# Kernel optimization log

Hardware: AMD Instinct MI355X
Metric: run time of the kernel (lower is better)

The kernel has to match this reference:

```python
import jax, jax.numpy as jnp
import numpy as np
from jax import lax


def setup_inputs() -> dict:
    key = jax.random.key(0)
    kx, kw = jax.random.split(key)
    x = jax.random.normal(kx, (8, 32, 16, 160, 160), dtype=jnp.float32)
    # xavier-normal-ish init (scale irrelevant to correctness testing)
    weights = jax.random.normal(kw, (32, 32, 1, 3, 3), dtype=jnp.float32) * 0.1
    return {"x": x, "weights": weights}


def reference(x, weights):
    # per-(out_ch, in_ch) scale: mean |w| over kernel dims (2,3,4), detached
    scale = lax.stop_gradient(jnp.mean(jnp.abs(weights), axis=(2, 3, 4), keepdims=True))
    binary_no_grad = scale * jnp.sign(weights)          # {+-scale}
    clipped = jnp.clip(weights, -1.0, 1.0)
    # straight-through estimator: value = binary_no_grad, grad flows via clipped
    binary_weights = lax.stop_gradient(binary_no_grad - clipped) + clipped
    out = lax.conv_general_dilated(
        x, binary_weights,
        window_strides=(1, 1, 1),
        padding=((0, 0), (1, 1), (1, 1)),
        rhs_dilation=(1, 1, 1),
        dimension_numbers=("NCDHW", "OIDHW", "NCDHW"),
        feature_group_count=1,
    )
    return out
```

## Files before the change

kernel.cpp:

```cpp
#include <hip/hip_runtime.h>
#include <stdint.h>


typedef _Float16 half8  __attribute__((ext_vector_type(8)));
typedef float    floatx4 __attribute__((ext_vector_type(4)));

#define DHW 409600
#define HW  25600
#define RING_SLOT_B 10240
#define RING_B      40960
#define LDS_TOTAL   61440

__device__ __forceinline__ int w1s(int w1) { return w1 ^ ((w1 >> 2) & 1); }
__device__ __forceinline__ int f2v(int w1) { return ((w1 >> 1) ^ (w1 >> 3)) & 3; }

typedef const __attribute__((address_space(1))) uint32_t* gas1;
typedef __attribute__((address_space(3))) uint32_t* las3;
__device__ __forceinline__ void gld16(const void* g, void* l) {
    __builtin_amdgcn_global_load_lds((gas1)g, (las3)l, 16, 0, 0);
}
#define VMCNT(N) do { asm volatile("s_waitcnt vmcnt(" #N ")" ::: "memory"); \
                      __builtin_amdgcn_sched_barrier(0); } while (0)
__device__ __forceinline__ void barrier_raw() {
    __builtin_amdgcn_sched_barrier(0);
    asm volatile("s_waitcnt lgkmcnt(0)" ::: "memory");
    __builtin_amdgcn_s_barrier();
    __builtin_amdgcn_sched_barrier(0);
}

__global__ void bnn_wprep_kernel(const float* __restrict__ w,
                                 _Float16* __restrict__ ws) {
    const int tid = threadIdx.x;
    #pragma unroll
    for (int p4 = 0; p4 < 4; ++p4) {
        const int oi = tid * 4 + p4;
        const int o  = oi >> 5;
        const int i  = oi & 31;
        const float* wp = w + oi * 9;
        float s = 0.f;
        #pragma unroll
        for (int t = 0; t < 9; ++t) s += fabsf(wp[t]);
        s *= (1.f / 9.f);
        const int l = ((i >> 3) << 4) | (o & 15);
        const int p = o >> 4;
        const int j = i & 7;
        #pragma unroll
        for (int t = 0; t < 9; ++t) {
            const float v  = wp[t];
            const float sg = (v > 0.f) ? 1.f : ((v < 0.f) ? -1.f : 0.f);
            ws[((t * 2 + p) * 64 + l) * 8 + j] = (_Float16)(s * sg);
        }
    }
}

__global__ __launch_bounds__(320, 3) void bnn_conv3d_dma(
        const float* __restrict__ x, const _Float16* __restrict__ ws,
        float* __restrict__ out) {
    __shared__ __align__(16) char lds[LDS_TOTAL];

    const int tid  = threadIdx.x;
    const int lane = tid & 63;
    const int wv   = tid >> 6;

    const int bid = blockIdx.x;
    const int hc  = bid & 3;
    const int d   = (bid >> 2) & 15;
    const int n   = bid >> 6;
    const int h0  = hc * 40;

    const float* qb[4];
    {
        const int chl = lane >> 3;
        const int wl  = (lane & 7) * 4;
        #pragma unroll
        for (int q = 0; q < 4; ++q)
            qb[q] = x + (size_t)(n * 32 + q * 8 + chl) * DHW + d * HW + wv * 32 + wl;
    }

    half8 wf0[9], wf1[9];
    {
        const half8* fb = (const half8*)ws;
        #pragma unroll
        for (int t = 0; t < 9; ++t) {
            wf0[t] = fb[(t * 2 + 0) * 64 + lane];
            wf1[t] = fb[(t * 2 + 1) * 64 + lane];
        }
    }
    asm volatile("s_waitcnt vmcnt(0)" ::: "memory");
    __builtin_amdgcn_sched_barrier(0);

    const int pcell = 32 * wv + (lane >> 1);
    const int w1p   = w1s(pcell);
    const int wloc  = w1p - wv * 32;
    const int chb   = (lane & 1) * 16;
    int soff[16];
    #pragma unroll
    for (int c = 0; c < 16; ++c) {
        const int ch = chb + c;
        soff[c] = (wv * 4 + (ch >> 3)) * 1024 + ((ch & 7) * 8 + (wloc >> 2)) * 16
                + (wloc & 3) * 4;
    }
    const int f2p = f2v(pcell);
    const int rb0 = pcell * 64 + ((((lane & 1) * 2)     ^ f2p) * 16);
    const int rb1 = pcell * 64 + ((((lane & 1) * 2 + 1) ^ f2p) * 16);

    const int s16 = lane & 15, kgr = lane >> 4;
    int rdo[2][3];
    #pragma unroll
    for (int gi = 0; gi < 2; ++gi)
        #pragma unroll
        for (int kw = 0; kw < 3; ++kw) {
            int wq = (2 * wv + gi) * 16 + s16 + kw - 1;
            wq = wq < 0 ? 0 : (wq > 159 ? 159 : wq);
            rdo[gi][kw] = (w1s(wq) * 32 + ((kgr ^ f2v(wq)) * 8)) * 2;
        }
    const bool okA = (wv * 32 + s16 - 1) >= 0;
    const bool okB = (wv * 32 + 16 + s16 + 1) < 160;
    float* ob = out + (size_t)(n * 32 + s16) * DHW + d * HW + wv * 32 + kgr * 4;

    auto DMA = [&](int r) {
        int h = h0 - 1 + r; h = h < 0 ? 0 : (h > 159 ? 159 : h);
        char* dst = lds + RING_B + wv * 4096;
        #pragma unroll
        for (int q = 0; q < 4; ++q)
            gld16(qb[q] + h * 160, dst + q * 1024);
        __builtin_amdgcn_sched_barrier(0);
    };
    auto PACK = [&](int r) {
        const int hr = h0 - 1 + r;
        const char* sl = lds + RING_B;
        char* rg = lds + (r & 3) * RING_SLOT_B;
        half8 o0 = {}, o1 = {};
        if (hr >= 0 && hr < 160) {
            float f[16];
            #pragma unroll
            for (int c = 0; c < 16; ++c) f[c] = *(const float*)(sl + soff[c]);
            #pragma unroll
            for (int c = 0; c < 8; ++c) { o0[c] = (_Float16)f[c]; o1[c] = (_Float16)f[c + 8]; }
        }
        *(half8*)(rg + rb0) = o0;
        *(half8*)(rg + rb1) = o1;
    };
    auto COMPUTE = [&](int t) {
        const half8 zh = {};
        #pragma unroll
        for (int gi = 0; gi < 2; ++gi) {
            floatx4 a0 = {0.f, 0.f, 0.f, 0.f};
            floatx4 a1 = {0.f, 0.f, 0.f, 0.f};
            #pragma unroll
            for (int kh = 0; kh < 3; ++kh) {
                const char* sb = lds + ((t + kh) & 3) * RING_SLOT_B;
                #pragma unroll
                for (int kw = 0; kw < 3; ++kw) {
                    half8 a = *(const half8*)(sb + rdo[gi][kw]);
                    if (gi == 0 && kw == 0) a = okA ? a : zh;
                    if (gi == 1 && kw == 2) a = okB ? a : zh;
                    const int tp = kh * 3 + kw;
                    a0 = __builtin_amdgcn_mfma_f32_16x16x32_f16(a, wf0[tp], a0, 0, 0, 0);
                    a1 = __builtin_amdgcn_mfma_f32_16x16x32_f16(a, wf1[tp], a1, 0, 0, 0);
                }
            }
            float* op = ob + (size_t)(h0 + t) * 160 + gi * 16;
            *(floatx4*)op = a0;
            *(floatx4*)(op + (size_t)16 * DHW) = a1;
        }
    };

    DMA(0);
    VMCNT(0); PACK(0); barrier_raw(); DMA(1);
    VMCNT(0); PACK(1); barrier_raw(); DMA(2);
    VMCNT(0); PACK(2); barrier_raw(); DMA(3); COMPUTE(0);
    for (int t = 1; t <= 38; ++t) {
        VMCNT(4); PACK(t + 2); barrier_raw(); DMA(t + 3); COMPUTE(t);
    }
    VMCNT(4); PACK(41); barrier_raw(); COMPUTE(39);
}

extern "C" void kernel_launch(void* const* d_in, const int* in_sizes, int n_in,
                              void* d_out, int out_size, void* d_ws, size_t ws_size,
                              hipStream_t stream) {
    const float* x = (const float*)d_in[0];
    const float* w = (const float*)d_in[1];
    float* out = (float*)d_out;
    _Float16* ws = (_Float16*)d_ws;
    bnn_wprep_kernel<<<dim3(1), dim3(256), 0, stream>>>(w, ws);
    bnn_conv3d_dma<<<dim3(512), dim3(320), 0, stream>>>(x, ws, out);
}
```

Measured before the change: 186.9 us.

## Compute two output rows per pipeline step with a six-slot row ring

After: 194.4 us. +4.0%, slower.

```diff
diff --git a/kernel.cpp b/kernel.cpp
--- a/kernel.cpp
+++ b/kernel.cpp
@@ -8,8 +8,10 @@
 #define DHW 409600
 #define HW  25600
 #define RING_SLOT_B 10240
-#define RING_B      40960
-#define LDS_TOTAL   61440
+#define RING_B      61440
+#define SCR_B       61440
+#define SCR_SLOT_B  20480
+#define LDS_TOTAL   102400
 
 __device__ __forceinline__ int w1s(int w1) { return w1 ^ ((w1 >> 2) & 1); }
 __device__ __forceinline__ int f2v(int w1) { return ((w1 >> 1) ^ (w1 >> 3)) & 3; }
@@ -53,7 +55,7 @@
     }
 }
 
-__global__ __launch_bounds__(320, 3) void bnn_conv3d_dma(
+__global__ __launch_bounds__(320) void bnn_conv3d_dma(
         const float* __restrict__ x, const _Float16* __restrict__ ws,
         float* __restrict__ out) {
     __shared__ __align__(16) char lds[LDS_TOTAL];
@@ -63,10 +65,10 @@
     const int wv   = tid >> 6;
 
     const int bid = blockIdx.x;
-    const int hc  = bid & 3;
-    const int d   = (bid >> 2) & 15;
-    const int n   = bid >> 6;
-    const int h0  = hc * 40;
+    const int hc  = bid & 1;
+    const int d   = (bid >> 1) & 15;
+    const int n   = bid >> 5;
+    const int h0  = hc * 80;
 
     const float* qb[4];
     {
@@ -118,62 +120,85 @@
     const bool okB = (wv * 32 + 16 + s16 + 1) < 160;
     float* ob = out + (size_t)(n * 32 + s16) * DHW + d * HW + wv * 32 + kgr * 4;
 
-    auto DMA = [&](int r) {
-        int h = h0 - 1 + r; h = h < 0 ? 0 : (h > 159 ? 159 : h);
-        char* dst = lds + RING_B + wv * 4096;
-        #pragma unroll
-        for (int q = 0; q < 4; ++q)
-            gld16(qb[q] + h * 160, dst + q * 1024);
+    auto DMA = [&](int u) {
+        #pragma unroll
+        for (int rr = 0; rr < 2; ++rr) {
+            int h = h0 - 1 + 2 * u + rr;
+            h = h < 0 ? 0 : (h > 159 ? 159 : h);
+            char* dst = lds + SCR_B + rr * SCR_SLOT_B + wv * 4096;
+            #pragma unroll
+            for (int q = 0; q < 4; ++q)
+                gld16(qb[q] + h * 160, dst + q * 1024);
+        }
         __builtin_amdgcn_sched_barrier(0);
     };
-    auto PACK = [&](int r) {
-        const int hr = h0 - 1 + r;
-        const char* sl = lds + RING_B;
-        char* rg = lds + (r & 3) * RING_SLOT_B;
-        half8 o0 = {}, o1 = {};
-        if (hr >= 0 && hr < 160) {
-            float f[16];
-            #pragma unroll
-            for (int c = 0; c < 16; ++c) f[c] = *(const float*)(sl + soff[c]);
-            #pragma unroll
-            for (int c = 0; c < 8; ++c) { o0[c] = (_Float16)f[c]; o1[c] = (_Float16)f[c + 8]; }
-        }
-        *(half8*)(rg + rb0) = o0;
-        *(half8*)(rg + rb1) = o1;
+    auto PACK = [&](int u) {
+        #pragma unroll
+        for (int rr = 0; rr < 2; ++rr) {
+            const int r  = 2 * u + rr;
+            const int hr = h0 - 1 + r;
+            const char* sl = lds + SCR_B + rr * SCR_SLOT_B;
+            char* rg = lds + (r % 6) * RING_SLOT_B;
+            half8 o0 = {}, o1 = {};
+            if (hr >= 0 && hr < 160) {
+                float f[16];
+                #pragma unroll
+                for (int c = 0; c < 16; ++c) f[c] = *(const float*)(sl + soff[c]);
+                #pragma unroll
+                for (int c = 0; c < 8; ++c) { o0[c] = (_Float16)f[c]; o1[c] = (_Float16)f[c + 8]; }
+            }
+            *(half8*)(rg + rb0) = o0;
+            *(half8*)(rg + rb1) = o1;
+        }
     };
     auto COMPUTE = [&](int t) {
         const half8 zh = {};
+        const floatx4 z4 = {0.f, 0.f, 0.f, 0.f};
         #pragma unroll
         for (int gi = 0; gi < 2; ++gi) {
-            floatx4 a0 = {0.f, 0.f, 0.f, 0.f};
-            floatx4 a1 = {0.f, 0.f, 0.f, 0.f};
+            floatx4 ac[2][2] = {{z4, z4}, {z4, z4}};
             #pragma unroll
-            for (int kh = 0; kh < 3; ++kh) {
-                const char* sb = lds + ((t + kh) & 3) * RING_SLOT_B;
+            for (int rr = 0; rr < 4; ++rr) {
+                const char* sb = lds + ((2 * t + rr) % 6) * RING_SLOT_B;
+                half8 av[3];
                 #pragma unroll
                 for (int kw = 0; kw < 3; ++kw) {
                     half8 a = *(const half8*)(sb + rdo[gi][kw]);
                     if (gi == 0 && kw == 0) a = okA ? a : zh;
                     if (gi == 1 && kw == 2) a = okB ? a : zh;
-                    const int tp = kh * 3 + kw;
-                    a0 = __builtin_amdgcn_mfma_f32_16x16x32_f16(a, wf0[tp], a0, 0, 0, 0);
-                    a1 = __builtin_amdgcn_mfma_f32_16x16x32_f16(a, wf1[tp], a1, 0, 0, 0);
+                    av[kw] = a;
+                }
+                #pragma unroll
+                for (int kw = 0; kw < 3; ++kw) {
+                    if (rr < 3) {
+                        const int tp = rr * 3 + kw;
+                        ac[0][0] = __builtin_amdgcn_mfma_f32_16x16x32_f16(av[kw], wf0[tp], ac[0][0], 0, 0, 0);
+                        ac[0][1] = __builtin_amdgcn_mfma_f32_16x16x32_f16(av[kw], wf1[tp], ac[0][1], 0, 0, 0);
+                    }
+                    if (rr >= 1) {
+                        const int tp = (rr - 1) * 3 + kw;
+                        ac[1][0] = __builtin_amdgcn_mfma_f32_16x16x32_f16(av[kw], wf0[tp], ac[1][0], 0, 0, 0);
+                        ac[1][1] = __builtin_amdgcn_mfma_f32_16x16x32_f16(av[kw], wf1[tp], ac[1][1], 0, 0, 0);
+                    }
                 }
             }
-            float* op = ob + (size_t)(h0 + t) * 160 + gi * 16;
-            *(floatx4*)op = a0;
-            *(floatx4*)(op + (size_t)16 * DHW) = a1;
+            #pragma unroll
+            for (int rl = 0; rl < 2; ++rl) {
+                float* op = ob + (size_t)(h0 + 2 * t + rl) * 160 + gi * 16;
+                *(floatx4*)op = ac[rl][0];
+                *(floatx4*)(op + (size_t)16 * DHW) = ac[rl][1];
+            }
         }
     };
 
     DMA(0);
     VMCNT(0); PACK(0); barrier_raw(); DMA(1);
     VMCNT(0); PACK(1); barrier_raw(); DMA(2);
-    VMCNT(0); PACK(2); barrier_raw(); DMA(3); COMPUTE(0);
+    COMPUTE(0);
     for (int t = 1; t <= 38; ++t) {
-        VMCNT(4); PACK(t + 2); barrier_raw(); DMA(t + 3); COMPUTE(t);
-    }
-    VMCNT(4); PACK(41); barrier_raw(); COMPUTE(39);
+        VMCNT(8); PACK(t + 1); barrier_raw(); DMA(t + 2); COMPUTE(t);
+    }
+    VMCNT(8); PACK(40); barrier_raw(); COMPUTE(39);
 }
 
 extern "C" void kernel_launch(void* const* d_in, const int* in_sizes, int n_in,
@@ -184,5 +209,5 @@
     float* out = (float*)d_out;
     _Float16* ws = (_Float16*)d_ws;
     bnn_wprep_kernel<<<dim3(1), dim3(256), 0, stream>>>(w, ws);
-    bnn_conv3d_dma<<<dim3(512), dim3(320), 0, stream>>>(x, ws, out);
-}
+    bnn_conv3d_dma<<<dim3(256), dim3(320), 0, stream>>>(x, ws, out);
+}
```
